# Kernel optimization log

Measured on AMD Instinct MI355X. Metric: run time of the kernel, lower is better.

The kernel has to match this reference:

```python
import jax, jax.numpy as jnp
import numpy as np

INF = 1000000000.0
TEMP = 0.1      # dsmax_temperature
THR = 0.2       # confidence threshold
BORDER = 2      # border_rm
H0C, W0C = 60, 80
H1C, W1C = 60, 80
SCALE = 8.0     # hw0_i[0]/hw0_c[0] = 480/60


def setup_inputs() -> dict:
    key = jax.random.key(0)
    k0, k1 = jax.random.split(key)
    N, C = 2, 256
    L = H0C * W0C
    S = H1C * W1C
    feat_c0 = jax.random.normal(k0, (N, L, C), jnp.float32)
    feat_c1 = jax.random.normal(k1, (N, S, C), jnp.float32)
    # padded masks: batch 0 full frame, batch 1 has a smaller valid region
    hi = jnp.arange(H0C)[None, :, None]
    wi = jnp.arange(W0C)[None, None, :]
    h0_valid = jnp.array([H0C, 52])[:, None, None]
    w0_valid = jnp.array([W0C, 72])[:, None, None]
    h1_valid = jnp.array([H1C, 56])[:, None, None]
    w1_valid = jnp.array([W1C, 76])[:, None, None]
    mask0 = (hi < h0_valid) & (wi < w0_valid)   # [N, H0C, W0C] bool
    mask1 = (hi < h1_valid) & (wi < w1_valid)   # [N, H1C, W1C] bool
    return {"feat_c0": feat_c0, "feat_c1": feat_c1, "mask0": mask0, "mask1": mask1}


def _border_valid(mask_hw, hc, wc, n):
    # valid = inside [BORDER, dim_valid - BORDER) per batch (separable in h and w)
    m = mask_hw.astype(jnp.int32)
    hs = jnp.max(jnp.sum(m, axis=1), axis=-1)   # [N] effective heights
    ws = jnp.max(jnp.sum(m, axis=-1), axis=-1)  # [N] effective widths
    hi = jnp.arange(hc)[None, :]
    wi = jnp.arange(wc)[None, :]
    vh = (hi >= BORDER) & (hi < (hs[:, None] - BORDER))  # [N, hc]
    vw = (wi >= BORDER) & (wi < (ws[:, None] - BORDER))  # [N, wc]
    return (vh[:, :, None] & vw[:, None, :]).reshape(n, hc * wc)  # [N, hc*wc]


def reference(feat_c0, feat_c1, mask0, mask1):
    N, L, C = feat_c0.shape
    S = feat_c1.shape[1]
    inv_sqrt_c = 1.0 / (C ** 0.5)
    f0 = feat_c0 * inv_sqrt_c
    f1 = feat_c1 * inv_sqrt_c
    sim = jnp.einsum("nlc,nsc->nls", f0, f1) / TEMP  # [N, L, S]
    mc0 = mask0.reshape(N, L)
    mc1 = mask1.reshape(N, S)
    sim = jnp.where(mc0[:, :, None] & mc1[:, None, :], sim, -INF)
    conf = jax.nn.softmax(sim, axis=1) * jax.nn.softmax(sim, axis=2)  # dual-softmax

    # threshold + padded border removal (separable per-batch border masks)
    valid0 = _border_valid(mask0, H0C, W0C, N)  # [N, L]
    valid1 = _border_valid(mask1, H1C, W1C, N)  # [N, S]
    mask = (conf > THR) & valid0[:, :, None] & valid1[:, None, :]

    # mutual nearest neighbor
    conf_max2 = jnp.max(conf, axis=2, keepdims=True)
    conf_max1 = jnp.max(conf, axis=1, keepdims=True)
    mask = mask & (conf == conf_max2) & (conf == conf_max1)

    # dense match extraction (fixed-shape analogue of torch.where gather)
    mask_v = jnp.any(mask, axis=2)                         # [N, L]
    j_ids = jnp.argmax(mask, axis=2).astype(jnp.int32)     # [N, L] (first True)
    mconf = jnp.take_along_axis(conf, j_ids[..., None].astype(jnp.int32), axis=2)[..., 0]
    mconf = mconf * mask_v                                 # zero where unmatched

    i_ids = jnp.arange(L, dtype=jnp.int32)
    pts0 = jnp.stack([i_ids % W0C, i_ids // W0C], axis=-1).astype(conf.dtype) * SCALE  # [L, 2]
    mkpts0 = jnp.broadcast_to(pts0[None], (N, L, 2))
    mkpts1 = jnp.stack([j_ids % W1C, j_ids // W1C], axis=-1).astype(conf.dtype) * SCALE  # [N, L, 2]
    return conf, mask_v, j_ids, mconf, mkpts0, mkpts1
```

## Files before the change

### kernel.cpp

```cpp
#include <hip/hip_runtime.h>

#define LD 4800
#define SD 4800
#define CD 256
#define H0 60
#define W0 80
#define NBATCH 2
#define THRV 0.2f
#define NEGINF (-1000000000.0f)
#define SIMSCALE 0.0390625f

typedef __attribute__((ext_vector_type(8))) short bf16x8;
typedef __attribute__((ext_vector_type(4))) float f32x4;
typedef __attribute__((ext_vector_type(4))) unsigned short u16x4;

__device__ __forceinline__ bool mask_is_u8(const void* m) {
  return ((const unsigned char*)m)[1] != 0;
}
__device__ __forceinline__ bool mask_at(const void* m, int idx, bool u8) {
  if (u8) return ((const unsigned char*)m)[idx] != 0;
  return ((const unsigned int*)m)[idx] != 0u;
}
__device__ __forceinline__ unsigned short f2bf(float x) {
  return (unsigned short)((__float_as_uint(x) + 0x8000u) >> 16);
}


__global__ void init_kernel(const void* __restrict__ m0, const void* __restrict__ m1,
                            unsigned* __restrict__ wszero, int* __restrict__ dims) {
  const int t = threadIdx.x;
  const int gid = blockIdx.x * 256 + t;
  for (int i = gid; i < 48000; i += gridDim.x * 256) wszero[i] = 0u;
  if (blockIdx.x != 0) return;

  const bool u8 = mask_is_u8(m0);
  __shared__ short cnt[160];
  if (t < NBATCH * W0) {
    int n = t / W0, w = t % W0, c = 0;
    for (int h = 0; h < H0; ++h) c += mask_at(m0, n * LD + h * W0 + w, u8) ? 1 : 0;
    cnt[t] = (short)c;
  }
  __syncthreads();
  if (t < NBATCH) { int mx = 0; for (int w = 0; w < W0; ++w) mx = max(mx, (int)cnt[t * W0 + w]); dims[0 + t] = mx; }
  __syncthreads();
  if (t < NBATCH * H0) {
    int n = t / H0, h = t % H0, c = 0;
    for (int w = 0; w < W0; ++w) c += mask_at(m0, n * LD + h * W0 + w, u8) ? 1 : 0;
    cnt[t] = (short)c;
  }
  __syncthreads();
  if (t < NBATCH) { int mx = 0; for (int h = 0; h < H0; ++h) mx = max(mx, (int)cnt[t * H0 + h]); dims[2 + t] = mx; }
  __syncthreads();
  if (t < NBATCH * W0) {
    int n = t / W0, w = t % W0, c = 0;
    for (int h = 0; h < H0; ++h) c += mask_at(m1, n * SD + h * W0 + w, u8) ? 1 : 0;
    cnt[t] = (short)c;
  }
  __syncthreads();
  if (t < NBATCH) { int mx = 0; for (int w = 0; w < W0; ++w) mx = max(mx, (int)cnt[t * W0 + w]); dims[4 + t] = mx; }
  __syncthreads();
  if (t < NBATCH * H0) {
    int n = t / H0, h = t % H0, c = 0;
    for (int w = 0; w < W0; ++w) c += mask_at(m1, n * SD + h * W0 + w, u8) ? 1 : 0;
    cnt[t] = (short)c;
  }
  __syncthreads();
  if (t < NBATCH) { int mx = 0; for (int h = 0; h < H0; ++h) mx = max(mx, (int)cnt[t * H0 + h]); dims[6 + t] = mx; }
}

__global__ __launch_bounds__(256)
void gemm_kernel(const float* __restrict__ f0, const float* __restrict__ f1,
                 const void* __restrict__ m0, const void* __restrict__ m1,
                 float* __restrict__ simout, float* __restrict__ rowsum,
                 float* __restrict__ colsum) {
  const int n  = blockIdx.z;
  const int br = blockIdx.y * 128;
  const int bs = blockIdx.x * 128;
  const int t = threadIdx.x;
  const int lane = t & 63, wv = t >> 6;
  const int wr = wv >> 1, wc = wv & 1;
  const int q = lane >> 4, c0 = lane & 15;

  __shared__ unsigned short As[128 * 40];
  __shared__ unsigned short Bs[128 * 40];

  const float* A = f0 + (size_t)n * LD * CD;
  const float* B = f1 + (size_t)n * SD * CD;

  f32x4 acc[4][4] = {};

  for (int k0 = 0; k0 < CD; k0 += 32) {
    __syncthreads();
#pragma unroll
    for (int i = 0; i < 4; ++i) {
      int e = (i * 256 + t) * 4;
      int row = e >> 5, k = e & 31;
      int gr = br + row; if (gr >= LD) gr = LD - 1;
      int gs = bs + row; if (gs >= SD) gs = SD - 1;
      f32x4 va = *(const f32x4*)(A + (size_t)gr * CD + (k0 + k));
      f32x4 vb = *(const f32x4*)(B + (size_t)gs * CD + (k0 + k));
      u16x4 ua = { f2bf(va.x), f2bf(va.y), f2bf(va.z), f2bf(va.w) };
      u16x4 ub = { f2bf(vb.x), f2bf(vb.y), f2bf(vb.z), f2bf(vb.w) };
      *(u16x4*)(As + row * 40 + k) = ua;
      *(u16x4*)(Bs + row * 40 + k) = ub;
    }
    __syncthreads();
    bf16x8 af[4], bfr[4];
#pragma unroll
    for (int m = 0; m < 4; ++m)
      af[m] = *(const bf16x8*)(As + (wr * 64 + m * 16 + c0) * 40 + q * 8);
#pragma unroll
    for (int m = 0; m < 4; ++m)
      bfr[m] = *(const bf16x8*)(Bs + (wc * 64 + m * 16 + c0) * 40 + q * 8);
#pragma unroll
    for (int m = 0; m < 4; ++m)
#pragma unroll
      for (int nn = 0; nn < 4; ++nn)
        acc[m][nn] = __builtin_amdgcn_mfma_f32_16x16x32_bf16(af[m], bfr[nn], acc[m][nn], 0, 0, 0);
  }

  const bool u8 = mask_is_u8(m0);
  int grow[16]; bool inrow[16], mrow[16];
#pragma unroll
  for (int m = 0; m < 4; ++m)
#pragma unroll
    for (int i = 0; i < 4; ++i) {
      int r = br + wr * 64 + m * 16 + q * 4 + i;
      int idx = m * 4 + i;
      grow[idx] = r;
      bool inb = r < LD;
      inrow[idx] = inb;
      mrow[idx] = inb && mask_at(m0, n * LD + (inb ? r : 0), u8);
    }
  int gcol[4]; bool incol[4], mcol[4];
#pragma unroll
  for (int nn = 0; nn < 4; ++nn) {
    int c = bs + wc * 64 + nn * 16 + c0;
    gcol[nn] = c;
    bool inb = c < SD;
    incol[nn] = inb;
    mcol[nn] = inb && mask_at(m1, n * SD + (inb ? c : 0), u8);
  }

  float rpart[16];
#pragma unroll
  for (int i = 0; i < 16; ++i) rpart[i] = 0.f;
  float cpart[4] = {0.f, 0.f, 0.f, 0.f};

#pragma unroll
  for (int m = 0; m < 4; ++m)
#pragma unroll
    for (int nn = 0; nn < 4; ++nn) {
      f32x4 a = acc[m][nn];
#pragma unroll
      for (int i = 0; i < 4; ++i) {
        int idx = m * 4 + i;
        float val = a[i] * SIMSCALE;
        bool v = mrow[idx] && mcol[nn];
        float e = v ? __expf(val) : 0.f;
        rpart[idx] += e;
        cpart[nn] += e;
        if (inrow[idx] && incol[nn])
          simout[((size_t)n * LD + grow[idx]) * SD + gcol[nn]] = v ? val : NEGINF;
      }
    }

#pragma unroll
  for (int idx = 0; idx < 16; ++idx) {
    float s = rpart[idx];
    s += __shfl_xor(s, 1); s += __shfl_xor(s, 2);
    s += __shfl_xor(s, 4); s += __shfl_xor(s, 8);
    if (c0 == 0 && inrow[idx]) atomicAdd(&rowsum[n * LD + grow[idx]], s);
  }
#pragma unroll
  for (int nn = 0; nn < 4; ++nn) {
    float s = cpart[nn];
    s += __shfl_xor(s, 16); s += __shfl_xor(s, 32);
    if (q == 0 && incol[nn]) atomicAdd(&colsum[n * SD + gcol[nn]], s);
  }
}

__global__ __launch_bounds__(256)
void conf_kernel(float* __restrict__ buf, const float* __restrict__ rowsum,
                 const float* __restrict__ colsum,
                 const void* __restrict__ m0, const void* __restrict__ m1,
                 unsigned* __restrict__ colmax, unsigned long long* __restrict__ rowbest) {
  const int n  = blockIdx.z;
  const int ro = blockIdx.x * 64;
  const int co = blockIdx.y * 256;
  const int t = threadIdx.x, lane = t & 63, wv = t >> 6;
  const bool u8 = mask_is_u8(m0);
  const int c = co + lane * 4;
  const bool colok = c < SD;
  const float invS = 1.0f / SD, invL = 1.0f / LD;

  f32x4 cinv = {0.f, 0.f, 0.f, 0.f};
  bool mc1v[4] = {false, false, false, false};
  if (colok) {
    f32x4 cs = *(const f32x4*)(colsum + n * SD + c);
    cinv.x = 1.0f / cs.x; cinv.y = 1.0f / cs.y;
    cinv.z = 1.0f / cs.z; cinv.w = 1.0f / cs.w;
#pragma unroll
    for (int j = 0; j < 4; ++j) mc1v[j] = mask_at(m1, n * SD + c + j, u8);
  }
  float cm[4] = {0.f, 0.f, 0.f, 0.f};

  for (int i = 0; i < 16; ++i) {
    const int r = ro + i * 4 + wv;
    const float rinv = 1.0f / rowsum[n * LD + r];
    const bool mc0r = mask_at(m0, n * LD + r, u8);
    unsigned long long key = 0ull;
    if (colok) {
      size_t off = ((size_t)n * LD + r) * SD + c;
      f32x4 sv = *(f32x4*)(buf + off);
      f32x4 cf;
      float best = -1.f; int bc = c;
#pragma unroll
      for (int j = 0; j < 4; ++j) {
        float e = __expf(sv[j]);
        float Aa = mc0r   ? e * rinv   : invS;
        float Bb = mc1v[j] ? e * cinv[j] : invL;
        float cv = Aa * Bb;
        cf[j] = cv;
        if (cv > best) { best = cv; bc = c + j; }
        cm[j] = fmaxf(cm[j], cv);
      }
      *(f32x4*)(buf + off) = cf;
      key = ((unsigned long long)__float_as_uint(best) << 32) | (unsigned)(~bc);
    }
#pragma unroll
    for (int d = 1; d < 64; d <<= 1) {
      unsigned long long ok = __shfl_xor(key, d);
      key = (ok > key) ? ok : key;
    }
    if (lane == 0) atomicMax(&rowbest[n * LD + r], key);
  }

  __shared__ unsigned shm[4][256];
#pragma unroll
  for (int j = 0; j < 4; ++j) shm[wv][lane * 4 + j] = colok ? __float_as_uint(cm[j]) : 0u;
  __syncthreads();
  {
    unsigned mx = max(max(shm[0][t], shm[1][t]), max(shm[2][t], shm[3][t]));
    int cc = co + t;
    if (cc < SD) atomicMax(&colmax[n * SD + cc], mx);
  }
}

__global__ void final_kernel(const unsigned long long* __restrict__ rowbest,
                             const unsigned* __restrict__ colmax,
                             const int* __restrict__ dims,
                             float* __restrict__ out) {
  const int n = blockIdx.y;
  const int l = blockIdx.x * 256 + threadIdx.x;
  if (l >= LD) return;
  unsigned long long key = rowbest[(size_t)n * LD + l];
  float rmax = __uint_as_float((unsigned)(key >> 32));
  int j = (int)(~(unsigned)(key & 0xFFFFFFFFull));
  if (j < 0 || j >= SD) j = 0;
  const int hs0 = dims[0 + n], ws0 = dims[2 + n], hs1 = dims[4 + n], ws1 = dims[6 + n];
  const int h = l / W0, w = l % W0;
  const bool v0 = (h >= 2) && (h < hs0 - 2) && (w >= 2) && (w < ws0 - 2);
  const int jh = j / W0, jw = j % W0;
  const bool v1 = (jh >= 2) && (jh < hs1 - 2) && (jw >= 2) && (jw < ws1 - 2);
  const float cmx = __uint_as_float(colmax[(size_t)n * SD + j]);
  const bool mv = (rmax > THRV) && v0 && v1 && (rmax == cmx);
  const int jid = mv ? j : 0;

  const size_t base = (size_t)NBATCH * LD * SD;
  const int NL = NBATCH * LD;
  out[base + (size_t)n * LD + l]            = mv ? 1.f : 0.f;
  out[base + NL + (size_t)n * LD + l]       = (float)jid;
  out[base + 2 * (size_t)NL + (size_t)n * LD + l] = mv ? rmax : 0.f;
  size_t mk0 = base + 3 * (size_t)NL + ((size_t)n * LD + l) * 2;
  out[mk0 + 0] = (float)(w * 8);
  out[mk0 + 1] = (float)(h * 8);
  size_t mk1 = base + 5 * (size_t)NL + ((size_t)n * LD + l) * 2;
  out[mk1 + 0] = (float)((jid % W0) * 8);
  out[mk1 + 1] = (float)((jid / W0) * 8);
}

extern "C" void kernel_launch(void* const* d_in, const int* in_sizes, int n_in,
                              void* d_out, int out_size, void* d_ws, size_t ws_size,
                              hipStream_t stream) {
  (void)in_sizes; (void)n_in; (void)out_size; (void)ws_size;
  const float* f0 = (const float*)d_in[0];
  const float* f1 = (const float*)d_in[1];
  const void*  m0 = d_in[2];
  const void*  m1 = d_in[3];
  float* out = (float*)d_out;
  char* ws = (char*)d_ws;

  float* rowsum = (float*)(ws);
  float* colsum = (float*)(ws + 38400);
  unsigned* colmax = (unsigned*)(ws + 76800);
  unsigned long long* rowbest = (unsigned long long*)(ws + 115200);
  int* dims = (int*)(ws + 192000);

  init_kernel<<<64, 256, 0, stream>>>(m0, m1, (unsigned*)ws, dims);
  gemm_kernel<<<dim3(38, 38, 2), 256, 0, stream>>>(f0, f1, m0, m1, out, rowsum, colsum);
  conf_kernel<<<dim3(75, 19, 2), 256, 0, stream>>>(out, rowsum, colsum, m0, m1, colmax, rowbest);
  final_kernel<<<dim3(19, 2), 256, 0, stream>>>(rowbest, colmax, dims, out);
}
```

Before: 464.0 us.

## Recompute similarity GEMM in two passes instead of storing and rereading sim matrix

Drops the intermediate similarity write and the separate conf pass. The GEMM now runs twice: the first pass accumulates row and column exp sums, and the second recomputes the scores, writes conf directly and does the row-best and column-max reductions in registers. Features are pre-converted to bf16 in a prep kernel so the GEMM can stream them into LDS with global_load_lds when the workspace is large enough. This trades a second GEMM for about 184 MB less traffic to and from the large output matrix. Removing the padded LDS stride may add bank conflicts.

```diff
diff --git a/kernel.cpp b/kernel.cpp
--- a/kernel.cpp
+++ b/kernel.cpp
@@ -5,74 +5,92 @@
 #define CD 256
 #define H0 60
 #define W0 80
-#define NBATCH 2
+#define NB 2
 #define THRV 0.2f
-#define NEGINF (-1000000000.0f)
 #define SIMSCALE 0.0390625f
+#define INVL (1.0f/4800.0f)
 
 typedef __attribute__((ext_vector_type(8))) short bf16x8;
 typedef __attribute__((ext_vector_type(4))) float f32x4;
 typedef __attribute__((ext_vector_type(4))) unsigned short u16x4;
+typedef __attribute__((ext_vector_type(8))) unsigned short u16x8;
+typedef unsigned long long ull;
 
 __device__ __forceinline__ bool mask_is_u8(const void* m) {
   return ((const unsigned char*)m)[1] != 0;
 }
 __device__ __forceinline__ bool mask_at(const void* m, int idx, bool u8) {
-  if (u8) return ((const unsigned char*)m)[idx] != 0;
-  return ((const unsigned int*)m)[idx] != 0u;
+  return u8 ? (((const unsigned char*)m)[idx] != 0)
+            : (((const unsigned int*)m)[idx] != 0u);
 }
 __device__ __forceinline__ unsigned short f2bf(float x) {
   return (unsigned short)((__float_as_uint(x) + 0x8000u) >> 16);
 }
 
 
-__global__ void init_kernel(const void* __restrict__ m0, const void* __restrict__ m1,
-                            unsigned* __restrict__ wszero, int* __restrict__ dims) {
+__global__ __launch_bounds__(256)
+void prep_kernel(const float* __restrict__ f0, const float* __restrict__ f1,
+                 const void* __restrict__ m0, const void* __restrict__ m1,
+                 unsigned short* __restrict__ fb0, unsigned short* __restrict__ fb1,
+                 unsigned* __restrict__ zws, int* __restrict__ dims, int do_conv) {
   const int t = threadIdx.x;
   const int gid = blockIdx.x * 256 + t;
-  for (int i = gid; i < 48000; i += gridDim.x * 256) wszero[i] = 0u;
-  if (blockIdx.x != 0) return;
-
-  const bool u8 = mask_is_u8(m0);
-  __shared__ short cnt[160];
-  if (t < NBATCH * W0) {
-    int n = t / W0, w = t % W0, c = 0;
-    for (int h = 0; h < H0; ++h) c += mask_at(m0, n * LD + h * W0 + w, u8) ? 1 : 0;
-    cnt[t] = (short)c;
-  }
-  __syncthreads();
-  if (t < NBATCH) { int mx = 0; for (int w = 0; w < W0; ++w) mx = max(mx, (int)cnt[t * W0 + w]); dims[0 + t] = mx; }
-  __syncthreads();
-  if (t < NBATCH * H0) {
-    int n = t / H0, h = t % H0, c = 0;
-    for (int w = 0; w < W0; ++w) c += mask_at(m0, n * LD + h * W0 + w, u8) ? 1 : 0;
-    cnt[t] = (short)c;
-  }
-  __syncthreads();
-  if (t < NBATCH) { int mx = 0; for (int h = 0; h < H0; ++h) mx = max(mx, (int)cnt[t * H0 + h]); dims[2 + t] = mx; }
-  __syncthreads();
-  if (t < NBATCH * W0) {
-    int n = t / W0, w = t % W0, c = 0;
-    for (int h = 0; h < H0; ++h) c += mask_at(m1, n * SD + h * W0 + w, u8) ? 1 : 0;
-    cnt[t] = (short)c;
-  }
-  __syncthreads();
-  if (t < NBATCH) { int mx = 0; for (int w = 0; w < W0; ++w) mx = max(mx, (int)cnt[t * W0 + w]); dims[4 + t] = mx; }
-  __syncthreads();
-  if (t < NBATCH * H0) {
-    int n = t / H0, h = t % H0, c = 0;
-    for (int w = 0; w < W0; ++w) c += mask_at(m1, n * SD + h * W0 + w, u8) ? 1 : 0;
-    cnt[t] = (short)c;
-  }
-  __syncthreads();
-  if (t < NBATCH) { int mx = 0; for (int h = 0; h < H0; ++h) mx = max(mx, (int)cnt[t * H0 + h]); dims[6 + t] = mx; }
-}
-
+  const int stride = gridDim.x * 256;
+  for (int i = gid; i < 48000; i += stride) zws[i] = 0u;
+  if (do_conv) {
+    for (int g = gid; g < 614400; g += stride) {
+      int gg = g; const float* src; unsigned short* dst;
+      if (gg < 307200) { src = f0; dst = fb0; } else { gg -= 307200; src = f1; dst = fb1; }
+      size_t off = (size_t)gg * 8;
+      f32x4 a = *(const f32x4*)(src + off);
+      f32x4 b = *(const f32x4*)(src + off + 4);
+      u16x8 o = { f2bf(a.x), f2bf(a.y), f2bf(a.z), f2bf(a.w),
+                  f2bf(b.x), f2bf(b.y), f2bf(b.z), f2bf(b.w) };
+      *(u16x8*)(dst + off) = o;
+    }
+  }
+  if (blockIdx.x < 4) {
+    const bool u8 = mask_is_u8(m0);
+    __shared__ short cnt[160];
+    const int s = blockIdx.x;
+    const void* mm = (s < 2) ? m0 : m1;
+    if (s == 0 || s == 2) {
+      if (t < NB * W0) {
+        int n = t / W0, w = t % W0, c = 0;
+        for (int h = 0; h < H0; ++h) c += mask_at(mm, n * LD + h * W0 + w, u8) ? 1 : 0;
+        cnt[t] = (short)c;
+      }
+      __syncthreads();
+      if (t < NB) {
+        int mx = 0;
+        for (int w = 0; w < W0; ++w) mx = max(mx, (int)cnt[t * W0 + w]);
+        dims[(s == 0 ? 0 : 4) + t] = mx;
+      }
+    } else {
+      if (t < NB * H0) {
+        int n = t / H0, h = t % H0, c = 0;
+        for (int w = 0; w < W0; ++w) c += mask_at(mm, n * LD + h * W0 + w, u8) ? 1 : 0;
+        cnt[t] = (short)c;
+      }
+      __syncthreads();
+      if (t < NB) {
+        int mx = 0;
+        for (int h = 0; h < H0; ++h) mx = max(mx, (int)cnt[t * H0 + h]);
+        dims[(s == 1 ? 2 : 6) + t] = mx;
+      }
+    }
+  }
+}
+
+template<int PASS, int GLL>
 __global__ __launch_bounds__(256)
-void gemm_kernel(const float* __restrict__ f0, const float* __restrict__ f1,
-                 const void* __restrict__ m0, const void* __restrict__ m1,
-                 float* __restrict__ simout, float* __restrict__ rowsum,
-                 float* __restrict__ colsum) {
+void gemm_fused(const unsigned short* __restrict__ fb0,
+                const unsigned short* __restrict__ fb1,
+                const float* __restrict__ f0, const float* __restrict__ f1,
+                const void* __restrict__ m0, const void* __restrict__ m1,
+                float* __restrict__ out, float* __restrict__ rowsum,
+                float* __restrict__ colsum, unsigned* __restrict__ colmax,
+                ull* __restrict__ rowbest) {
   const int n  = blockIdx.z;
   const int br = blockIdx.y * 128;
   const int bs = blockIdx.x * 128;
@@ -81,42 +99,75 @@
   const int wr = wv >> 1, wc = wv & 1;
   const int q = lane >> 4, c0 = lane & 15;
 
-  __shared__ unsigned short As[128 * 40];
-  __shared__ unsigned short Bs[128 * 40];
-
-  const float* A = f0 + (size_t)n * LD * CD;
-  const float* B = f1 + (size_t)n * SD * CD;
+  __shared__ unsigned short As[128 * 32];
+  __shared__ unsigned short Bs[128 * 32];
 
   f32x4 acc[4][4] = {};
 
-  for (int k0 = 0; k0 < CD; k0 += 32) {
-    __syncthreads();
-#pragma unroll
-    for (int i = 0; i < 4; ++i) {
-      int e = (i * 256 + t) * 4;
-      int row = e >> 5, k = e & 31;
-      int gr = br + row; if (gr >= LD) gr = LD - 1;
-      int gs = bs + row; if (gs >= SD) gs = SD - 1;
-      f32x4 va = *(const f32x4*)(A + (size_t)gr * CD + (k0 + k));
-      f32x4 vb = *(const f32x4*)(B + (size_t)gs * CD + (k0 + k));
-      u16x4 ua = { f2bf(va.x), f2bf(va.y), f2bf(va.z), f2bf(va.w) };
-      u16x4 ub = { f2bf(vb.x), f2bf(vb.y), f2bf(vb.z), f2bf(vb.w) };
-      *(u16x4*)(As + row * 40 + k) = ua;
-      *(u16x4*)(Bs + row * 40 + k) = ub;
-    }
-    __syncthreads();
-    bf16x8 af[4], bfr[4];
-#pragma unroll
-    for (int m = 0; m < 4; ++m)
-      af[m] = *(const bf16x8*)(As + (wr * 64 + m * 16 + c0) * 40 + q * 8);
-#pragma unroll
-    for (int m = 0; m < 4; ++m)
-      bfr[m] = *(const bf16x8*)(Bs + (wc * 64 + m * 16 + c0) * 40 + q * 8);
-#pragma unroll
-    for (int m = 0; m < 4; ++m)
-#pragma unroll
-      for (int nn = 0; nn < 4; ++nn)
-        acc[m][nn] = __builtin_amdgcn_mfma_f32_16x16x32_bf16(af[m], bfr[nn], acc[m][nn], 0, 0, 0);
+  if constexpr (GLL) {
+    const unsigned short* Ab = fb0 + (size_t)n * LD * CD;
+    const unsigned short* Bb = fb1 + (size_t)n * SD * CD;
+    const int kk = (t & 3) * 8;
+    const int r0 = t >> 2;
+    const int gr0 = min(br + r0, LD - 1),      gs0 = min(bs + r0, SD - 1);
+    const int gr1 = min(br + r0 + 64, LD - 1), gs1 = min(bs + r0 + 64, SD - 1);
+    for (int k0 = 0; k0 < CD; k0 += 32) {
+      __syncthreads();
+      __builtin_amdgcn_global_load_lds(
+          (const __attribute__((address_space(1))) void*)(Ab + (size_t)gr0 * CD + k0 + kk),
+          (__attribute__((address_space(3))) void*)(As + wv * 512), 16, 0, 0);
+      __builtin_amdgcn_global_load_lds(
+          (const __attribute__((address_space(1))) void*)(Ab + (size_t)gr1 * CD + k0 + kk),
+          (__attribute__((address_space(3))) void*)(As + 2048 + wv * 512), 16, 0, 0);
+      __builtin_amdgcn_global_load_lds(
+          (const __attribute__((address_space(1))) void*)(Bb + (size_t)gs0 * CD + k0 + kk),
+          (__attribute__((address_space(3))) void*)(Bs + wv * 512), 16, 0, 0);
+      __builtin_amdgcn_global_load_lds(
+          (const __attribute__((address_space(1))) void*)(Bb + (size_t)gs1 * CD + k0 + kk),
+          (__attribute__((address_space(3))) void*)(Bs + 2048 + wv * 512), 16, 0, 0);
+      __syncthreads();
+      bf16x8 af[4], bfr[4];
+#pragma unroll
+      for (int m = 0; m < 4; ++m) {
+        af[m]  = *(const bf16x8*)(As + (wr * 64 + m * 16 + c0) * 32 + q * 8);
+        bfr[m] = *(const bf16x8*)(Bs + (wc * 64 + m * 16 + c0) * 32 + q * 8);
+      }
+#pragma unroll
+      for (int m = 0; m < 4; ++m)
+#pragma unroll
+        for (int nn = 0; nn < 4; ++nn)
+          acc[m][nn] = __builtin_amdgcn_mfma_f32_16x16x32_bf16(af[m], bfr[nn], acc[m][nn], 0, 0, 0);
+    }
+  } else {
+    const float* A = f0 + (size_t)n * LD * CD;
+    const float* B = f1 + (size_t)n * SD * CD;
+    for (int k0 = 0; k0 < CD; k0 += 32) {
+      __syncthreads();
+#pragma unroll
+      for (int i = 0; i < 4; ++i) {
+        int e = (i * 256 + t) * 4;
+        int row = e >> 5, k = e & 31;
+        int gr = min(br + row, LD - 1), gs = min(bs + row, SD - 1);
+        f32x4 va = *(const f32x4*)(A + (size_t)gr * CD + k0 + k);
+        f32x4 vb = *(const f32x4*)(B + (size_t)gs * CD + k0 + k);
+        u16x4 ua = { f2bf(va.x), f2bf(va.y), f2bf(va.z), f2bf(va.w) };
+        u16x4 ub = { f2bf(vb.x), f2bf(vb.y), f2bf(vb.z), f2bf(vb.w) };
+        *(u16x4*)(As + row * 32 + k) = ua;
+        *(u16x4*)(Bs + row * 32 + k) = ub;
+      }
+      __syncthreads();
+      bf16x8 af[4], bfr[4];
+#pragma unroll
+      for (int m = 0; m < 4; ++m) {
+        af[m]  = *(const bf16x8*)(As + (wr * 64 + m * 16 + c0) * 32 + q * 8);
+        bfr[m] = *(const bf16x8*)(Bs + (wc * 64 + m * 16 + c0) * 32 + q * 8);
+      }
+#pragma unroll
+      for (int m = 0; m < 4; ++m)
+#pragma unroll
+        for (int nn = 0; nn < 4; ++nn)
+          acc[m][nn] = __builtin_amdgcn_mfma_f32_16x16x32_bf16(af[m], bfr[nn], acc[m][nn], 0, 0, 0);
+    }
   }
 
   const bool u8 = mask_is_u8(m0);
@@ -125,8 +176,8 @@
   for (int m = 0; m < 4; ++m)
 #pragma unroll
     for (int i = 0; i < 4; ++i) {
+      int idx = m * 4 + i;
       int r = br + wr * 64 + m * 16 + q * 4 + i;
-      int idx = m * 4 + i;
       grow[idx] = r;
       bool inb = r < LD;
       inrow[idx] = inb;
@@ -142,119 +193,105 @@
     mcol[nn] = inb && mask_at(m1, n * SD + (inb ? c : 0), u8);
   }
 
-  float rpart[16];
-#pragma unroll
-  for (int i = 0; i < 16; ++i) rpart[i] = 0.f;
-  float cpart[4] = {0.f, 0.f, 0.f, 0.f};
-
-#pragma unroll
-  for (int m = 0; m < 4; ++m)
+  if constexpr (PASS == 0) {
+    float rpart[16];
+#pragma unroll
+    for (int i = 0; i < 16; ++i) rpart[i] = 0.f;
+    float cpart[4] = {0.f, 0.f, 0.f, 0.f};
+#pragma unroll
+    for (int m = 0; m < 4; ++m)
+#pragma unroll
+      for (int nn = 0; nn < 4; ++nn) {
+        f32x4 a = acc[m][nn];
+#pragma unroll
+        for (int i = 0; i < 4; ++i) {
+          int idx = m * 4 + i;
+          float val = a[i] * SIMSCALE;
+          bool v = mrow[idx] && mcol[nn];
+          float e = v ? __expf(val) : 0.f;
+          rpart[idx] += e;
+          cpart[nn] += e;
+        }
+      }
+#pragma unroll
+    for (int idx = 0; idx < 16; ++idx) {
+      float s = rpart[idx];
+      s += __shfl_xor(s, 1); s += __shfl_xor(s, 2);
+      s += __shfl_xor(s, 4); s += __shfl_xor(s, 8);
+      if (c0 == 0 && inrow[idx]) atomicAdd(&rowsum[n * LD + grow[idx]], s);
+    }
 #pragma unroll
     for (int nn = 0; nn < 4; ++nn) {
-      f32x4 a = acc[m][nn];
-#pragma unroll
-      for (int i = 0; i < 4; ++i) {
-        int idx = m * 4 + i;
-        float val = a[i] * SIMSCALE;
-        bool v = mrow[idx] && mcol[nn];
-        float e = v ? __expf(val) : 0.f;
-        rpart[idx] += e;
-        cpart[nn] += e;
-        if (inrow[idx] && incol[nn])
-          simout[((size_t)n * LD + grow[idx]) * SD + gcol[nn]] = v ? val : NEGINF;
-      }
-    }
-
-#pragma unroll
-  for (int idx = 0; idx < 16; ++idx) {
-    float s = rpart[idx];
-    s += __shfl_xor(s, 1); s += __shfl_xor(s, 2);
-    s += __shfl_xor(s, 4); s += __shfl_xor(s, 8);
-    if (c0 == 0 && inrow[idx]) atomicAdd(&rowsum[n * LD + grow[idx]], s);
-  }
-#pragma unroll
-  for (int nn = 0; nn < 4; ++nn) {
-    float s = cpart[nn];
-    s += __shfl_xor(s, 16); s += __shfl_xor(s, 32);
-    if (q == 0 && incol[nn]) atomicAdd(&colsum[n * SD + gcol[nn]], s);
-  }
-}
-
-__global__ __launch_bounds__(256)
-void conf_kernel(float* __restrict__ buf, const float* __restrict__ rowsum,
-                 const float* __restrict__ colsum,
-                 const void* __restrict__ m0, const void* __restrict__ m1,
-                 unsigned* __restrict__ colmax, unsigned long long* __restrict__ rowbest) {
-  const int n  = blockIdx.z;
-  const int ro = blockIdx.x * 64;
-  const int co = blockIdx.y * 256;
-  const int t = threadIdx.x, lane = t & 63, wv = t >> 6;
-  const bool u8 = mask_is_u8(m0);
-  const int c = co + lane * 4;
-  const bool colok = c < SD;
-  const float invS = 1.0f / SD, invL = 1.0f / LD;
-
-  f32x4 cinv = {0.f, 0.f, 0.f, 0.f};
-  bool mc1v[4] = {false, false, false, false};
-  if (colok) {
-    f32x4 cs = *(const f32x4*)(colsum + n * SD + c);
-    cinv.x = 1.0f / cs.x; cinv.y = 1.0f / cs.y;
-    cinv.z = 1.0f / cs.z; cinv.w = 1.0f / cs.w;
-#pragma unroll
-    for (int j = 0; j < 4; ++j) mc1v[j] = mask_at(m1, n * SD + c + j, u8);
-  }
-  float cm[4] = {0.f, 0.f, 0.f, 0.f};
-
-  for (int i = 0; i < 16; ++i) {
-    const int r = ro + i * 4 + wv;
-    const float rinv = 1.0f / rowsum[n * LD + r];
-    const bool mc0r = mask_at(m0, n * LD + r, u8);
-    unsigned long long key = 0ull;
-    if (colok) {
-      size_t off = ((size_t)n * LD + r) * SD + c;
-      f32x4 sv = *(f32x4*)(buf + off);
-      f32x4 cf;
-      float best = -1.f; int bc = c;
-#pragma unroll
-      for (int j = 0; j < 4; ++j) {
-        float e = __expf(sv[j]);
-        float Aa = mc0r   ? e * rinv   : invS;
-        float Bb = mc1v[j] ? e * cinv[j] : invL;
-        float cv = Aa * Bb;
-        cf[j] = cv;
-        if (cv > best) { best = cv; bc = c + j; }
-        cm[j] = fmaxf(cm[j], cv);
-      }
-      *(f32x4*)(buf + off) = cf;
-      key = ((unsigned long long)__float_as_uint(best) << 32) | (unsigned)(~bc);
-    }
-#pragma unroll
-    for (int d = 1; d < 64; d <<= 1) {
-      unsigned long long ok = __shfl_xor(key, d);
-      key = (ok > key) ? ok : key;
-    }
-    if (lane == 0) atomicMax(&rowbest[n * LD + r], key);
-  }
-
-  __shared__ unsigned shm[4][256];
-#pragma unroll
-  for (int j = 0; j < 4; ++j) shm[wv][lane * 4 + j] = colok ? __float_as_uint(cm[j]) : 0u;
-  __syncthreads();
-  {
-    unsigned mx = max(max(shm[0][t], shm[1][t]), max(shm[2][t], shm[3][t]));
-    int cc = co + t;
-    if (cc < SD) atomicMax(&colmax[n * SD + cc], mx);
-  }
-}
-
-__global__ void final_kernel(const unsigned long long* __restrict__ rowbest,
+      float s = cpart[nn];
+      s += __shfl_xor(s, 16); s += __shfl_xor(s, 32);
+      if (q == 0 && incol[nn]) atomicAdd(&colsum[n * SD + gcol[nn]], s);
+    }
+  } else {
+    float rinv[16];
+#pragma unroll
+    for (int idx = 0; idx < 16; ++idx)
+      rinv[idx] = 1.0f / rowsum[n * LD + (inrow[idx] ? grow[idx] : 0)];
+    float cinv[4];
+#pragma unroll
+    for (int nn = 0; nn < 4; ++nn)
+      cinv[nn] = 1.0f / colsum[n * SD + (incol[nn] ? gcol[nn] : 0)];
+
+    ull rkey[16];
+#pragma unroll
+    for (int i = 0; i < 16; ++i) rkey[i] = 0ull;
+    float cmax[4] = {0.f, 0.f, 0.f, 0.f};
+
+#pragma unroll
+    for (int m = 0; m < 4; ++m)
+#pragma unroll
+      for (int nn = 0; nn < 4; ++nn) {
+        f32x4 a = acc[m][nn];
+#pragma unroll
+        for (int i = 0; i < 4; ++i) {
+          int idx = m * 4 + i;
+          float val = a[i] * SIMSCALE;
+          bool v = mrow[idx] && mcol[nn];
+          float e = v ? __expf(val) : 0.f;
+          float Aa = mrow[idx] ? e * rinv[idx] : INVL;
+          float Bb = mcol[nn] ? e * cinv[nn]  : INVL;
+          float cv = Aa * Bb;
+          bool ok = inrow[idx] && incol[nn];
+          if (ok) {
+            out[((size_t)n * LD + grow[idx]) * SD + gcol[nn]] = cv;
+            cmax[nn] = fmaxf(cmax[nn], cv);
+            ull key = ((ull)__float_as_uint(cv) << 32) | (unsigned)(~gcol[nn]);
+            if (key > rkey[idx]) rkey[idx] = key;
+          }
+        }
+      }
+#pragma unroll
+    for (int idx = 0; idx < 16; ++idx) {
+      ull key = rkey[idx];
+#pragma unroll
+      for (int d = 1; d < 16; d <<= 1) {
+        ull ok2 = __shfl_xor(key, d);
+        key = (ok2 > key) ? ok2 : key;
+      }
+      if (c0 == 0 && inrow[idx]) atomicMax(&rowbest[n * LD + grow[idx]], key);
+    }
+#pragma unroll
+    for (int nn = 0; nn < 4; ++nn) {
+      float s = cmax[nn];
+      s = fmaxf(s, __shfl_xor(s, 16));
+      s = fmaxf(s, __shfl_xor(s, 32));
+      if (q == 0 && incol[nn]) atomicMax(&colmax[n * SD + gcol[nn]], __float_as_uint(s));
+    }
+  }
+}
+
+__global__ void final_kernel(const ull* __restrict__ rowbest,
                              const unsigned* __restrict__ colmax,
                              const int* __restrict__ dims,
                              float* __restrict__ out) {
   const int n = blockIdx.y;
   const int l = blockIdx.x * 256 + threadIdx.x;
   if (l >= LD) return;
-  unsigned long long key = rowbest[(size_t)n * LD + l];
+  ull key = rowbest[(size_t)n * LD + l];
   float rmax = __uint_as_float((unsigned)(key >> 32));
   int j = (int)(~(unsigned)(key & 0xFFFFFFFFull));
   if (j < 0 || j >= SD) j = 0;
@@ -267,10 +304,10 @@
   const bool mv = (rmax > THRV) && v0 && v1 && (rmax == cmx);
   const int jid = mv ? j : 0;
 
-  const size_t base = (size_t)NBATCH * LD * SD;
-  const int NL = NBATCH * LD;
-  out[base + (size_t)n * LD + l]            = mv ? 1.f : 0.f;
-  out[base + NL + (size_t)n * LD + l]       = (float)jid;
+  const size_t base = (size_t)NB * LD * SD;
+  const int NL = NB * LD;
+  out[base + (size_t)n * LD + l]                  = mv ? 1.f : 0.f;
+  out[base + NL + (size_t)n * LD + l]             = (float)jid;
   out[base + 2 * (size_t)NL + (size_t)n * LD + l] = mv ? rmax : 0.f;
   size_t mk0 = base + 3 * (size_t)NL + ((size_t)n * LD + l) * 2;
   out[mk0 + 0] = (float)(w * 8);
@@ -283,7 +320,7 @@
 extern "C" void kernel_launch(void* const* d_in, const int* in_sizes, int n_in,
                               void* d_out, int out_size, void* d_ws, size_t ws_size,
                               hipStream_t stream) {
-  (void)in_sizes; (void)n_in; (void)out_size; (void)ws_size;
+  (void)in_sizes; (void)n_in; (void)out_size;
   const float* f0 = (const float*)d_in[0];
   const float* f1 = (const float*)d_in[1];
   const void*  m0 = d_in[2];
@@ -291,14 +328,31 @@
   float* out = (float*)d_out;
   char* ws = (char*)d_ws;
 
-  float* rowsum = (float*)(ws);
-  float* colsum = (float*)(ws + 38400);
-  unsigned* colmax = (unsigned*)(ws + 76800);
-  unsigned long long* rowbest = (unsigned long long*)(ws + 115200);
-  int* dims = (int*)(ws + 192000);
-
-  init_kernel<<<64, 256, 0, stream>>>(m0, m1, (unsigned*)ws, dims);
-  gemm_kernel<<<dim3(38, 38, 2), 256, 0, stream>>>(f0, f1, m0, m1, out, rowsum, colsum);
-  conf_kernel<<<dim3(75, 19, 2), 256, 0, stream>>>(out, rowsum, colsum, m0, m1, colmax, rowbest);
+  const size_t FB_BYTES = (size_t)NB * LD * CD * 2;
+  const bool gll = ws_size >= 2 * FB_BYTES + 192032;
+
+  unsigned short* fb0 = gll ? (unsigned short*)ws : nullptr;
+  unsigned short* fb1 = gll ? (unsigned short*)(ws + FB_BYTES) : nullptr;
+  char* sums = gll ? (ws + 2 * FB_BYTES) : ws;
+
+  float* rowsum = (float*)sums;
+  float* colsum = (float*)(sums + 38400);
+  unsigned* colmax = (unsigned*)(sums + 76800);
+  ull* rowbest = (ull*)(sums + 115200);
+  int* dims = (int*)(sums + 192000);
+
+  prep_kernel<<<512, 256, 0, stream>>>(f0, f1, m0, m1, fb0, fb1,
+                                       (unsigned*)sums, dims, gll ? 1 : 0);
+  if (gll) {
+    gemm_fused<0, 1><<<dim3(38, 38, 2), 256, 0, stream>>>(
+        fb0, fb1, f0, f1, m0, m1, out, rowsum, colsum, colmax, rowbest);
+    gemm_fused<1, 1><<<dim3(38, 38, 2), 256, 0, stream>>>(
+        fb0, fb1, f0, f1, m0, m1, out, rowsum, colsum, colmax, rowbest);
+  } else {
+    gemm_fused<0, 0><<<dim3(38, 38, 2), 256, 0, stream>>>(
+        fb0, fb1, f0, f1, m0, m1, out, rowsum, colsum, colmax, rowbest);
+    gemm_fused<1, 0><<<dim3(38, 38, 2), 256, 0, stream>>>(
+        fb0, fb1, f0, f1, m0, m1, out, rowsum, colsum, colmax, rowbest);
+  }
   final_kernel<<<dim3(19, 2), 256, 0, stream>>>(rowbest, colmax, dims, out);
 }
```

Result: faster. 419.1 us (-9.7%).
